# Kernel tuning notes

Measured on AMD Instinct MI355X. Metric: run time of the kernel, lower is better.

## Reference

```python
import jax, jax.numpy as jnp
import numpy as np

EMBED_DIM = 768
NUM_HEADS = 12
HEAD_DIM = EMBED_DIM // NUM_HEADS
MLP_RATIO = 4.0
HIDDEN_DIM = int(EMBED_DIM * MLP_RATIO)
B, N = 8, 1024


def setup_inputs() -> dict:
    key = jax.random.key(0)
    ks = jax.random.split(key, 12)
    d = EMBED_DIM
    h = HIDDEN_DIM
    s = lambda fan_in: 1.0 / np.sqrt(fan_in)
    return {
        "x": jax.random.normal(ks[0], (B, N, d), dtype=jnp.float32),
        "ln1_w": jnp.ones((d,), jnp.float32),
        "ln1_b": jnp.zeros((d,), jnp.float32),
        "qkv_w": jax.random.normal(ks[1], (3 * d, d), jnp.float32) * s(d),
        "qkv_b": jnp.zeros((3 * d,), jnp.float32),
        "proj_w": jax.random.normal(ks[2], (d, d), jnp.float32) * s(d),
        "proj_b": jnp.zeros((d,), jnp.float32),
        "ln2_w": jnp.ones((d,), jnp.float32),
        "ln2_b": jnp.zeros((d,), jnp.float32),
        "fc1_w": jax.random.normal(ks[3], (h, d), jnp.float32) * s(d),
        "fc1_b": jnp.zeros((h,), jnp.float32),
        "fc2_w": jax.random.normal(ks[4], (d, h), jnp.float32) * s(h),
        "fc2_b": jnp.zeros((d,), jnp.float32),
    }


def _layernorm(x, w, b, eps=1e-5):
    mu = jnp.mean(x, axis=-1, keepdims=True)
    var = jnp.var(x, axis=-1, keepdims=True)
    return (x - mu) * jax.lax.rsqrt(var + eps) * w + b


def _attention(x, qkv_w, qkv_b, proj_w, proj_b):
    b, n, c = x.shape
    qkv = x @ qkv_w.T + qkv_b  # [B, N, 3C]
    qkv = qkv.reshape(b, n, 3, NUM_HEADS, HEAD_DIM)
    q, k, v = jnp.moveaxis(qkv, 2, 0)  # each [B, N, H, Dh]
    scale = HEAD_DIM ** -0.5
    attn = jnp.einsum("bqhd,bkhd->bhqk", q, k) * scale  # [B, H, N, N]
    attn = jax.nn.softmax(attn, axis=-1)
    out = jnp.einsum("bhqk,bkhd->bqhd", attn, v).reshape(b, n, c)
    return out @ proj_w.T + proj_b


def reference(x, ln1_w, ln1_b, qkv_w, qkv_b, proj_w, proj_b,
              ln2_w, ln2_b, fc1_w, fc1_b, fc2_w, fc2_b):
    x = x + _attention(_layernorm(x, ln1_w, ln1_b), qkv_w, qkv_b, proj_w, proj_b)
    h = _layernorm(x, ln2_w, ln2_b)
    h = jax.nn.gelu(h @ fc1_w.T + fc1_b, approximate=False)
    x = x + (h @ fc2_w.T + fc2_b)
    return x
```

## Files before the change

kernel.cpp:

```cpp
#include <hip/hip_runtime.h>
#include <hip/hip_bf16.h>
#include <math.h>

typedef __attribute__((ext_vector_type(8))) short bf16x8;
typedef __attribute__((ext_vector_type(4))) float f32x4;
typedef unsigned short ushort_t;

#define GLOAD(srcp, dstp) __builtin_amdgcn_global_load_lds((const __attribute__((address_space(1))) void*)(srcp), (__attribute__((address_space(3))) void*)(dstp), 16, 0, 0)

__device__ inline ushort_t f2bfn(float f){
  union{ __bf16 h; ushort_t u; } c;
  c.h = (__bf16)f;
  return c.u;
}

__global__ __launch_bounds__(256) void cvt_all(const float* __restrict__ q, const float* __restrict__ p,
                                               const float* __restrict__ f1, const float* __restrict__ f2w,
                                               ushort_t* __restrict__ dq, ushort_t* __restrict__ dp,
                                               ushort_t* __restrict__ d1, ushort_t* __restrict__ d2){
  int i4 = blockIdx.x*256 + threadIdx.x;
  const float* src; ushort_t* dst; int off;
  if(i4 < 442368){ src=q;  dst=dq; off=i4; }
  else if(i4 < 589824){ src=p;  dst=dp; off=i4-442368; }
  else if(i4 < 1179648){ src=f1; dst=d1; off=i4-589824; }
  else { src=f2w; dst=d2; off=i4-1179648; }
  int i = off*4;
  float4 v = *(const float4*)(src+i);
  ushort4 o; o.x=f2bfn(v.x); o.y=f2bfn(v.y); o.z=f2bfn(v.z); o.w=f2bfn(v.w);
  *(ushort4*)(dst+i) = o;
}

__global__ __launch_bounds__(192) void ln_kernel(const float* __restrict__ x, const float* __restrict__ w,
                                                 const float* __restrict__ b, ushort_t* __restrict__ out){
  int row = blockIdx.x, t = threadIdx.x;
  const float4 v = *(const float4*)(x + (size_t)row*768 + t*4);
  float s  = v.x+v.y+v.z+v.w;
  float s2 = v.x*v.x+v.y*v.y+v.z*v.z+v.w*v.w;
  for(int m=1;m<64;m<<=1){ s += __shfl_xor(s,m,64); s2 += __shfl_xor(s2,m,64); }
  __shared__ float ls[3], ls2[3];
  int wv_ = t>>6;
  if((t&63)==0){ ls[wv_]=s; ls2[wv_]=s2; }
  __syncthreads();
  s = ls[0]+ls[1]+ls[2]; s2 = ls2[0]+ls2[1]+ls2[2];
  float mu = s*(1.f/768.f);
  float var = s2*(1.f/768.f) - mu*mu;
  float rs = rsqrtf(var + 1e-5f);
  float4 wv4 = *(const float4*)(w + t*4);
  float4 bv4 = *(const float4*)(b + t*4);
  ushort4 o;
  o.x = f2bfn((v.x-mu)*rs*wv4.x + bv4.x);
  o.y = f2bfn((v.y-mu)*rs*wv4.y + bv4.y);
  o.z = f2bfn((v.z-mu)*rs*wv4.z + bv4.z);
  o.w = f2bfn((v.w-mu)*rs*wv4.w + bv4.w);
  *(ushort4*)(out + (size_t)row*768 + t*4) = o;
}

template<int EPI>
__device__ __forceinline__
void gemm8_body(const ushort_t* __restrict__ A, const ushort_t* __restrict__ BT,
                const float* __restrict__ bias, void* __restrict__ out,
                int K, int Nout, int nBN)
{
  __shared__ ushort_t lds[65536];
  ushort_t* As = lds;
  ushort_t* Bs = lds + 32768;
  const int tid = threadIdx.x;
  const int lane = tid & 63, wid = tid >> 6;
  const int wm = wid >> 2, wn = wid & 3;
  const int fq = lane >> 4, fr = lane & 15;

  const int nwg = (int)gridDim.x;
  const int bid = (int)blockIdx.x;
  const int wg = (bid & 7)*(nwg>>3) + (bid>>3);
  const int bm0 = (wg / nBN) << 8;
  const int bn0 = (wg % nBN) << 8;

  const int srow0 = tid >> 2;
  const int srow1 = 128 + srow0;
  const int sgc = ((tid & 3) ^ ((srow0 >> 1) & 3)) << 3;

  auto stageA = [&](int slot, int tile, int kh){
    const int k0 = (tile<<6) + (kh<<5);
    GLOAD(A + (size_t)(bm0 + srow0)*K + k0 + sgc, As + slot*8192 + (wid*64)*8);
    GLOAD(A + (size_t)(bm0 + srow1)*K + k0 + sgc, As + slot*8192 + (512 + wid*64)*8);
  };
  auto stageB = [&](int slot, int tile, int kh){
    const int k0 = (tile<<6) + (kh<<5);
    GLOAD(BT + (size_t)(bn0 + srow0)*K + k0 + sgc, Bs + slot*8192 + (wid*64)*8);
    GLOAD(BT + (size_t)(bn0 + srow1)*K + k0 + sgc, Bs + slot*8192 + (512 + wid*64)*8);
  };

  int aoff[8], boff[4];
  #pragma unroll
  for(int m=0;m<8;m++){ int r = wm*128 + m*16 + fr; aoff[m] = r*32 + ((fq ^ ((r>>1)&3))<<3); }
  #pragma unroll
  for(int n=0;n<4;n++){ int r = wn*64  + n*16 + fr; boff[n] = r*32 + ((fq ^ ((r>>1)&3))<<3); }

  f32x4 acc[8][4];
  #pragma unroll
  for(int m=0;m<8;m++)
    #pragma unroll
    for(int n=0;n<4;n++) acc[m][n] = (f32x4){0.f,0.f,0.f,0.f};

  const int NT = K >> 6;
  stageA(0,0,0); stageB(0,0,0);
  stageA(1,0,1); stageB(1,0,1);
  stageA(2,1,0); stageB(2,1,0);
  asm volatile("s_waitcnt vmcnt(4)" ::: "memory");
  __builtin_amdgcn_s_barrier();

  for(int g=0; g<NT; ++g){
    const int par = g & 1;
    const int sl0 = par*2, sl1 = par*2 + 1;
    const int osl1 = (par^1)*2 + 1;
    bf16x8 a[8], b0, b1;

    #pragma unroll
    for(int m=0;m<8;m++) a[m] = *(const bf16x8*)(As + sl0*8192 + aoff[m]);
    b0 = *(const bf16x8*)(Bs + sl0*8192 + boff[0]);
    b1 = *(const bf16x8*)(Bs + sl0*8192 + boff[1]);
    if(g+1 < NT) stageA(osl1, g+1, 1);
    __builtin_amdgcn_s_barrier();
    asm volatile("s_waitcnt lgkmcnt(0)" ::: "memory");
    __builtin_amdgcn_s_setprio(1);
    #pragma unroll
    for(int m=0;m<8;m++){
      acc[m][0] = __builtin_amdgcn_mfma_f32_16x16x32_bf16(a[m], b0, acc[m][0], 0,0,0);
      acc[m][1] = __builtin_amdgcn_mfma_f32_16x16x32_bf16(a[m], b1, acc[m][1], 0,0,0);
    }
    __builtin_amdgcn_s_setprio(0);

    b0 = *(const bf16x8*)(Bs + sl0*8192 + boff[2]);
    b1 = *(const bf16x8*)(Bs + sl0*8192 + boff[3]);
    if(g+1 < NT) stageB(osl1, g+1, 1);
    __builtin_amdgcn_s_barrier();
    asm volatile("s_waitcnt lgkmcnt(0)" ::: "memory");
    __builtin_amdgcn_s_setprio(1);
    #pragma unroll
    for(int m=0;m<8;m++){
      acc[m][2] = __builtin_amdgcn_mfma_f32_16x16x32_bf16(a[m], b0, acc[m][2], 0,0,0);
      acc[m][3] = __builtin_amdgcn_mfma_f32_16x16x32_bf16(a[m], b1, acc[m][3], 0,0,0);
    }
    __builtin_amdgcn_s_setprio(0);
    if(g+1 < NT){ asm volatile("s_waitcnt vmcnt(8)" ::: "memory"); }
    else        { asm volatile("s_waitcnt vmcnt(0)" ::: "memory"); }
    __builtin_amdgcn_s_barrier();

    #pragma unroll
    for(int m=0;m<8;m++) a[m] = *(const bf16x8*)(As + sl1*8192 + aoff[m]);
    b0 = *(const bf16x8*)(Bs + sl1*8192 + boff[0]);
    b1 = *(const bf16x8*)(Bs + sl1*8192 + boff[1]);
    if(g+2 < NT) stageA(sl0, g+2, 0);
    __builtin_amdgcn_s_barrier();
    asm volatile("s_waitcnt lgkmcnt(0)" ::: "memory");
    __builtin_amdgcn_s_setprio(1);
    #pragma unroll
    for(int m=0;m<8;m++){
      acc[m][0] = __builtin_amdgcn_mfma_f32_16x16x32_bf16(a[m], b0, acc[m][0], 0,0,0);
      acc[m][1] = __builtin_amdgcn_mfma_f32_16x16x32_bf16(a[m], b1, acc[m][1], 0,0,0);
    }
    __builtin_amdgcn_s_setprio(0);

    b0 = *(const bf16x8*)(Bs + sl1*8192 + boff[2]);
    b1 = *(const bf16x8*)(Bs + sl1*8192 + boff[3]);
    if(g+2 < NT) stageB(sl0, g+2, 0);
    __builtin_amdgcn_s_barrier();
    asm volatile("s_waitcnt lgkmcnt(0)" ::: "memory");
    __builtin_amdgcn_s_setprio(1);
    #pragma unroll
    for(int m=0;m<8;m++){
      acc[m][2] = __builtin_amdgcn_mfma_f32_16x16x32_bf16(a[m], b0, acc[m][2], 0,0,0);
      acc[m][3] = __builtin_amdgcn_mfma_f32_16x16x32_bf16(a[m], b1, acc[m][3], 0,0,0);
    }
    __builtin_amdgcn_s_setprio(0);
    if(g+2 < NT)      { asm volatile("s_waitcnt vmcnt(8)" ::: "memory"); }
    else if(g+1 < NT) { asm volatile("s_waitcnt vmcnt(4)" ::: "memory"); }
    else              { asm volatile("s_waitcnt vmcnt(0)" ::: "memory"); }
    __builtin_amdgcn_s_barrier();
  }

  __syncthreads();
  const float qscale = 0.18033688f;
  const bool isQ = (EPI==0) && (bn0 < 768);
  #pragma unroll
  for(int m=0;m<8;m++){
    #pragma unroll
    for(int n=0;n<4;n++){
      int colL = wn*64 + n*16 + fr;
      float bv = bias[bn0 + colL];
      #pragma unroll
      for(int j=0;j<4;j++){
        int rowL = wm*128 + m*16 + fq*4 + j;
        float v = acc[m][n][j] + bv;
        if constexpr(EPI==2){
          float u = fminf(v*(1.0f + 0.044715f*v*v), 40.f);
          float e = exp2f(2.3020052f*u);
          v = v*e/(1.0f+e);
        }
        if(isQ) v *= qscale;
        lds[rowL*256 + (colL ^ (((rowL>>2)&3)<<4))] = f2bfn(v);
      }
    }
  }
  __syncthreads();
  const bool isV = (EPI==0) && (bn0 >= 1536);
  if(!isV){
    #pragma unroll 4
    for(int p=0;p<16;p++){
      int flat = tid + p*512;
      int row = flat>>5;
      int c8  = flat&31;
      int col = c8*8;
      bf16x8 v8 = *(const bf16x8*)&lds[row*256 + (col ^ (((row>>2)&3)<<4))];
      int rg = bm0 + row;
      if constexpr(EPI==0){
        int colg = bn0 + col;
        int which = colg >= 768 ? 1 : 0;
        int rem = colg - which*768;
        int hh = rem>>6, dh = rem&63;
        int bb = rg>>10, np = rg&1023;
        *(bf16x8*)&((ushort_t*)out)[(((size_t)(which*96 + bb*12 + hh)*1024 + np)<<6) + dh] = v8;
      } else {
        *(bf16x8*)&((ushort_t*)out)[(size_t)rg*(size_t)Nout + bn0 + col] = v8;
      }
    }
  } else {
    #pragma unroll 4
    for(int p=0;p<16;p++){
      int flat = tid + p*512;
      int dL = flat>>5;
      int t8 = (flat&31)*8;
      ushort_t tmp[8];
      #pragma unroll
      for(int i=0;i<8;i++){
        int row = t8 + i;
        tmp[i] = lds[row*256 + (dL ^ (((row>>2)&3)<<4))];
      }
      int dg = bn0 - 1536 + dL;
      int hh = dg>>6, dh = dg&63;
      int tok0 = bm0 + t8;
      int bb = tok0>>10, np = tok0&1023;
      *(bf16x8*)&((ushort_t*)out)[((size_t)(192 + bb*12 + hh)*65536) + dh*1024 + np] = *(bf16x8*)tmp;
    }
  }
}

__global__ __launch_bounds__(512, 2)
void qkv_gemm8(const ushort_t* __restrict__ A, const ushort_t* __restrict__ BT,
               const float* __restrict__ bias, void* __restrict__ out, int K, int Nout, int nBN)
{ gemm8_body<0>(A, BT, bias, out, K, Nout, nBN); }

__global__ __launch_bounds__(512, 2)
void fc1_gemm8(const ushort_t* __restrict__ A, const ushort_t* __restrict__ BT,
               const float* __restrict__ bias, void* __restrict__ out, int K, int Nout, int nBN)
{ gemm8_body<2>(A, BT, bias, out, K, Nout, nBN); }

__device__ __forceinline__
void gemm_body_epi1(const ushort_t* __restrict__ A, const ushort_t* __restrict__ BT,
                    const float* __restrict__ bias, const float* __restrict__ resid,
                    float* __restrict__ out, int K, int nBN)
{
  __shared__ ushort_t Asm[4][64*32];
  __shared__ ushort_t Bsm[4][128*32];
  const int nwg = (int)gridDim.x;
  const int bid = (int)blockIdx.x;
  const int wg = (bid & 7)*(nwg>>3) + (bid>>3);
  const int bm0 = (wg / nBN) * 64;
  const int bn0 = (wg % nBN) * 128;
  const int tid = threadIdx.x;
  const int lane = tid & 63;
  const int wid = tid >> 6;
  const int wn = wid;
  const int fq = lane>>4, fr = lane&15;

  const int rA = tid>>2;
  const int cAs = ((tid&3) ^ ((rA>>1)&3))<<3;
  const int r0 = wid*32 + (lane>>2);
  const int r1 = r0 + 16;
  const int cBs = ((lane&3) ^ ((r0>>1)&3))<<3;

  f32x4 acc[4][2];
  for(int m=0;m<4;m++) for(int n=0;n<2;n++) acc[m][n] = (f32x4){0.f,0.f,0.f,0.f};

  auto STAGE = [&](int buf, int k0){
    GLOAD(A  + (size_t)(bm0+rA)*K + k0 + cAs, &Asm[buf][wid*512]);
    GLOAD(BT + (size_t)(bn0+r0)*K + k0 + cBs, &Bsm[buf][(wid*2)*512]);
    GLOAD(BT + (size_t)(bn0+r1)*K + k0 + cBs, &Bsm[buf][(wid*2+1)*512]);
  };

  int aoff[4], boff[2];
  #pragma unroll
  for(int m=0;m<4;m++){ int r = m*16 + fr; aoff[m] = r*32 + ((fq ^ ((r>>1)&3))<<3); }
  #pragma unroll
  for(int n=0;n<2;n++){ int r = wn*32 + n*16 + fr; boff[n] = r*32 + ((fq ^ ((r>>1)&3))<<3); }

  const int NT = K>>5;
  STAGE(0, 0);
  STAGE(1, 32);
  STAGE(2, 64);
  asm volatile("s_waitcnt vmcnt(6)" ::: "memory");
  __builtin_amdgcn_s_barrier();

  int cur = 0;
  for(int kt=0; kt<NT; ++kt){
    if(kt+3 < NT) STAGE((cur+3)&3, (kt+3)<<5);
    bf16x8 af[4], bfr[2];
    #pragma unroll
    for(int m=0;m<4;m++)
      af[m] = *(const bf16x8*)(&Asm[cur][aoff[m]]);
    #pragma unroll
    for(int n=0;n<2;n++)
      bfr[n] = *(const bf16x8*)(&Bsm[cur][boff[n]]);
    #pragma unroll
    for(int m=0;m<4;m++)
      #pragma unroll
      for(int n=0;n<2;n++)
        acc[m][n] = __builtin_amdgcn_mfma_f32_16x16x32_bf16(af[m], bfr[n], acc[m][n], 0,0,0);
    if(kt+1 < NT){
      if(kt+3 < NT)      { asm volatile("s_waitcnt vmcnt(6)" ::: "memory"); }
      else if(kt+2 < NT) { asm volatile("s_waitcnt vmcnt(3)" ::: "memory"); }
      else               { asm volatile("s_waitcnt vmcnt(0)" ::: "memory"); }
      __builtin_amdgcn_s_barrier();
    }
    cur = (cur+1)&3;
  }

  for(int m=0;m<4;m++){
    int row0 = bm0 + m*16 + fq*4;
    for(int n=0;n<2;n++){
      int col = bn0 + wn*32 + n*16 + fr;
      float bv = bias[col];
      for(int j=0;j<4;j++){
        int r = row0 + j;
        float v = acc[m][n][j] + bv + resid[(size_t)r*768 + col];
        out[(size_t)r*768 + col] = v;
      }
    }
  }
}

__global__ __launch_bounds__(256)
void proj_gemm(const ushort_t* __restrict__ A, const ushort_t* __restrict__ BT,
               const float* __restrict__ bias, const float* __restrict__ resid,
               float* __restrict__ out, int K, int nBN)
{ gemm_body_epi1(A, BT, bias, resid, out, K, nBN); }

__global__ __launch_bounds__(256)
void fc2_gemm(const ushort_t* __restrict__ A, const ushort_t* __restrict__ BT,
              const float* __restrict__ bias, const float* __restrict__ resid,
              float* __restrict__ out, int K, int nBN)
{ gemm_body_epi1(A, BT, bias, resid, out, K, nBN); }

__global__ __launch_bounds__(256)
void attn_kernel(const ushort_t* __restrict__ qkv, ushort_t* __restrict__ outp)
{
  __shared__ ushort_t Ksm[2][64*72];
  __shared__ ushort_t Vt[2][64*72];
  __shared__ ushort_t Psm[4][16*72];
  const int bh = blockIdx.y;
  const int q0 = blockIdx.x*64;
  const int tid = threadIdx.x, lane = tid&63, wid = tid>>6;
  const int fq = lane>>4, fr = lane&15;
  const ushort_t* Qb = qkv + ((size_t)bh*1024)*64;
  const ushort_t* Kb = qkv + ((size_t)(96 + bh)*1024)*64;
  const ushort_t* Vb = qkv + ((size_t)(192 + bh))*65536;

  bf16x8 ones;
  #pragma unroll
  for(int i=0;i<8;i++) ones[i] = (short)0x3F80;

  bf16x8 qf[2];
  {
    int qr = q0 + wid*16 + fr;
    qf[0] = *(const bf16x8*)(Qb + (size_t)qr*64 +      fq*8);
    qf[1] = *(const bf16x8*)(Qb + (size_t)qr*64 + 32 + fq*8);
  }
  f32x4 o[4];
  for(int dt=0;dt<4;dt++) o[dt] = (f32x4){0.f,0.f,0.f,0.f};
  float lrun[4];
  for(int j=0;j<4;j++) lrun[j]=0.f;

  const int sr = tid>>3, sc = (tid&7)*8;

  bf16x8 k0r = *(const bf16x8*)(Kb + (size_t)sr*64 + sc);
  bf16x8 k1r = *(const bf16x8*)(Kb + (size_t)(sr+32)*64 + sc);
  bf16x8 v0r = *(const bf16x8*)(Vb + (size_t)sr*1024 + sc);
  bf16x8 v1r = *(const bf16x8*)(Vb + (size_t)(sr+32)*1024 + sc);
  *(bf16x8*)(Ksm[0] + sr*72 + sc)      = k0r;
  *(bf16x8*)(Ksm[0] + (sr+32)*72 + sc) = k1r;
  *(bf16x8*)(Vt[0]  + sr*72 + sc)      = v0r;
  *(bf16x8*)(Vt[0]  + (sr+32)*72 + sc) = v1r;

  int cur = 0;
  for(int kt=0; kt<16; kt++){
    __syncthreads();
    if(kt+1 < 16){
      int kv1 = (kt+1)*64;
      k0r = *(const bf16x8*)(Kb + (size_t)(kv1+sr)*64 + sc);
      k1r = *(const bf16x8*)(Kb + (size_t)(kv1+sr+32)*64 + sc);
      v0r = *(const bf16x8*)(Vb + (size_t)sr*1024 + kv1 + sc);
      v1r = *(const bf16x8*)(Vb + (size_t)(sr+32)*1024 + kv1 + sc);
    }

    f32x4 s[4];
    for(int ct=0;ct<4;ct++){
      bf16x8 kf0 = *(const bf16x8*)(Ksm[cur] + (ct*16 + fr)*72 +      fq*8);
      bf16x8 kf1 = *(const bf16x8*)(Ksm[cur] + (ct*16 + fr)*72 + 32 + fq*8);
      f32x4 z = (f32x4){0.f,0.f,0.f,0.f};
      z = __builtin_amdgcn_mfma_f32_16x16x32_bf16(qf[0], kf0, z, 0,0,0);
      z = __builtin_amdgcn_mfma_f32_16x16x32_bf16(qf[1], kf1, z, 0,0,0);
      s[ct] = z;
    }

    #pragma unroll
    for(int ct=0;ct<4;ct++){
      #pragma unroll
      for(int j=0;j<4;j++){
        float p = exp2f(s[ct][j]);
        int g = (ct*2 + (fr>>3)) ^ fq;
        Psm[wid][(fq*4 + j)*72 + g*8 + (fr&7)] = f2bfn(p);
      }
    }

    bf16x8 pf[2];
    {
      int key = (fr>>2)&3;
      pf[0] = *(const bf16x8*)(&Psm[wid][fr*72 + ((0*4+fq)^key)*8]);
      pf[1] = *(const bf16x8*)(&Psm[wid][fr*72 + ((1*4+fq)^key)*8]);
    }
    f32x4 o5 = (f32x4){0.f,0.f,0.f,0.f};
    o5 = __builtin_amdgcn_mfma_f32_16x16x32_bf16(pf[0], ones, o5, 0,0,0);
    o5 = __builtin_amdgcn_mfma_f32_16x16x32_bf16(pf[1], ones, o5, 0,0,0);
    #pragma unroll
    for(int j=0;j<4;j++) lrun[j] += o5[j];

    for(int dt=0;dt<4;dt++){
      for(int kc=0;kc<2;kc++){
        bf16x8 vf = *(const bf16x8*)(Vt[cur] + (dt*16 + fr)*72 + kc*32 + fq*8);
        o[dt] = __builtin_amdgcn_mfma_f32_16x16x32_bf16(pf[kc], vf, o[dt], 0,0,0);
      }
    }

    if(kt+1 < 16){
      *(bf16x8*)(Ksm[cur^1] + sr*72 + sc)      = k0r;
      *(bf16x8*)(Ksm[cur^1] + (sr+32)*72 + sc) = k1r;
      *(bf16x8*)(Vt[cur^1]  + sr*72 + sc)      = v0r;
      *(bf16x8*)(Vt[cur^1]  + (sr+32)*72 + sc) = v1r;
    }
    cur ^= 1;
  }

  int b = bh/12, h = bh%12;
  for(int dt=0;dt<4;dt++){
    for(int j=0;j<4;j++){
      int qr = q0 + wid*16 + fq*4 + j;
      float v = o[dt][j] / lrun[j];
      outp[(size_t)(b*1024 + qr)*768 + h*64 + dt*16 + fr] = f2bfn(v);
    }
  }
}

extern "C" void kernel_launch(void* const* d_in, const int* in_sizes, int n_in,
                              void* d_out, int out_size, void* d_ws, size_t ws_size,
                              hipStream_t stream)
{
  const float* x     = (const float*)d_in[0];
  const float* ln1w  = (const float*)d_in[1];
  const float* ln1b  = (const float*)d_in[2];
  const float* qkvw  = (const float*)d_in[3];
  const float* qkvb  = (const float*)d_in[4];
  const float* projw = (const float*)d_in[5];
  const float* projb = (const float*)d_in[6];
  const float* ln2w  = (const float*)d_in[7];
  const float* ln2b  = (const float*)d_in[8];
  const float* fc1w  = (const float*)d_in[9];
  const float* fc1b  = (const float*)d_in[10];
  const float* fc2w  = (const float*)d_in[11];
  const float* fc2b  = (const float*)d_in[12];

  char* ws = (char*)d_ws;
  size_t off = 0;
  auto alloc = [&](size_t bytes){ char* p = ws + off; off += (bytes + 255) & ~255ULL; return p; };
  ushort_t* wq = (ushort_t*)alloc((size_t)2304*768*2);
  ushort_t* wp = (ushort_t*)alloc((size_t)768*768*2);
  ushort_t* w1 = (ushort_t*)alloc((size_t)3072*768*2);
  ushort_t* w2 = (ushort_t*)alloc((size_t)768*3072*2);
  ushort_t* lnbuf  = (ushort_t*)alloc((size_t)8192*768*2);
  ushort_t* qkvbuf = (ushort_t*)alloc((size_t)3*96*1024*64*2);
  ushort_t* attno  = (ushort_t*)alloc((size_t)8192*768*2);
  ushort_t* hbuf   = qkvbuf;
  float* x1 = (float*)d_out;

  cvt_all<<<6912, 256, 0, stream>>>(qkvw, projw, fc1w, fc2w, wq, wp, w1, w2);
  ln_kernel<<<8192, 192, 0, stream>>>(x, ln1w, ln1b, lnbuf);
  qkv_gemm8<<<288, 512, 0, stream>>>(lnbuf, wq, qkvb, qkvbuf, 768, 2304, 9);
  attn_kernel<<<dim3(16,96), 256, 0, stream>>>(qkvbuf, attno);
  proj_gemm<<<768, 256, 0, stream>>>(attno, wp, projb, x, x1, 768, 6);
  ln_kernel<<<8192, 192, 0, stream>>>(x1, ln2w, ln2b, lnbuf);
  fc1_gemm8<<<384, 512, 0, stream>>>(lnbuf, w1, fc1b, hbuf, 768, 3072, 12);
  fc2_gemm<<<768, 256, 0, stream>>>(hbuf, w2, fc2b, x1, (float*)d_out, 3072, 6);
}
```

Baseline: 310.8 us.

## Halve GEMM LDS footprint with two-slot staging and split epilogue

Shrinks the shared-memory buffer for the QKV/FC1 GEMM from 128KB to 64KB. It drops the four-slot, two-tile-deep prefetch ring in favour of two fixed slots, each refilled once per iteration with a full vmcnt(0) wait. The epilogue now writes its bf16 tile through LDS in two 128-row halves so it fits the smaller buffer. The aim is to let two 512-thread workgroups share a CU (matching launch_bounds(512,2)), at the cost of a shallower prefetch that can expose global-load latency, plus extra barriers in the epilogue.

```diff
diff --git a/kernel.cpp b/kernel.cpp
--- a/kernel.cpp
+++ b/kernel.cpp
@@ -61,9 +61,9 @@
                 const float* __restrict__ bias, void* __restrict__ out,
                 int K, int Nout, int nBN)
 {
-  __shared__ ushort_t lds[65536];
+  __shared__ ushort_t lds[32768];
   ushort_t* As = lds;
-  ushort_t* Bs = lds + 32768;
+  ushort_t* Bs = lds + 16384;
   const int tid = threadIdx.x;
   const int lane = tid & 63, wid = tid >> 6;
   const int wm = wid >> 2, wn = wid & 3;
@@ -105,21 +105,17 @@
   const int NT = K >> 6;
   stageA(0,0,0); stageB(0,0,0);
   stageA(1,0,1); stageB(1,0,1);
-  stageA(2,1,0); stageB(2,1,0);
   asm volatile("s_waitcnt vmcnt(4)" ::: "memory");
   __builtin_amdgcn_s_barrier();
 
   for(int g=0; g<NT; ++g){
-    const int par = g & 1;
-    const int sl0 = par*2, sl1 = par*2 + 1;
-    const int osl1 = (par^1)*2 + 1;
     bf16x8 a[8], b0, b1;
 
     #pragma unroll
-    for(int m=0;m<8;m++) a[m] = *(const bf16x8*)(As + sl0*8192 + aoff[m]);
-    b0 = *(const bf16x8*)(Bs + sl0*8192 + boff[0]);
-    b1 = *(const bf16x8*)(Bs + sl0*8192 + boff[1]);
-    if(g+1 < NT) stageA(osl1, g+1, 1);
+    for(int m=0;m<8;m++) a[m] = *(const bf16x8*)(As + aoff[m]);
+    b0 = *(const bf16x8*)(Bs + boff[0]);
+    b1 = *(const bf16x8*)(Bs + boff[1]);
+    if(g >= 1){ stageA(1, g, 1); stageB(1, g, 1); }
     __builtin_amdgcn_s_barrier();
     asm volatile("s_waitcnt lgkmcnt(0)" ::: "memory");
     __builtin_amdgcn_s_setprio(1);
@@ -130,9 +126,8 @@
     }
     __builtin_amdgcn_s_setprio(0);
 
-    b0 = *(const bf16x8*)(Bs + sl0*8192 + boff[2]);
-    b1 = *(const bf16x8*)(Bs + sl0*8192 + boff[3]);
-    if(g+1 < NT) stageB(osl1, g+1, 1);
+    b0 = *(const bf16x8*)(Bs + boff[2]);
+    b1 = *(const bf16x8*)(Bs + boff[3]);
     __builtin_amdgcn_s_barrier();
     asm volatile("s_waitcnt lgkmcnt(0)" ::: "memory");
     __builtin_amdgcn_s_setprio(1);
@@ -142,15 +137,14 @@
       acc[m][3] = __builtin_amdgcn_mfma_f32_16x16x32_bf16(a[m], b1, acc[m][3], 0,0,0);
     }
     __builtin_amdgcn_s_setprio(0);
-    if(g+1 < NT){ asm volatile("s_waitcnt vmcnt(8)" ::: "memory"); }
-    else        { asm volatile("s_waitcnt vmcnt(0)" ::: "memory"); }
-    __builtin_amdgcn_s_barrier();
-
-    #pragma unroll
-    for(int m=0;m<8;m++) a[m] = *(const bf16x8*)(As + sl1*8192 + aoff[m]);
-    b0 = *(const bf16x8*)(Bs + sl1*8192 + boff[0]);
-    b1 = *(const bf16x8*)(Bs + sl1*8192 + boff[1]);
-    if(g+2 < NT) stageA(sl0, g+2, 0);
+    asm volatile("s_waitcnt vmcnt(0)" ::: "memory");
+    __builtin_amdgcn_s_barrier();
+
+    #pragma unroll
+    for(int m=0;m<8;m++) a[m] = *(const bf16x8*)(As + 8192 + aoff[m]);
+    b0 = *(const bf16x8*)(Bs + 8192 + boff[0]);
+    b1 = *(const bf16x8*)(Bs + 8192 + boff[1]);
+    if(g+1 < NT){ stageA(0, g+1, 0); stageB(0, g+1, 0); }
     __builtin_amdgcn_s_barrier();
     asm volatile("s_waitcnt lgkmcnt(0)" ::: "memory");
     __builtin_amdgcn_s_setprio(1);
@@ -161,9 +155,8 @@
     }
     __builtin_amdgcn_s_setprio(0);
 
-    b0 = *(const bf16x8*)(Bs + sl1*8192 + boff[2]);
-    b1 = *(const bf16x8*)(Bs + sl1*8192 + boff[3]);
-    if(g+2 < NT) stageB(sl0, g+2, 0);
+    b0 = *(const bf16x8*)(Bs + 8192 + boff[2]);
+    b1 = *(const bf16x8*)(Bs + 8192 + boff[3]);
     __builtin_amdgcn_s_barrier();
     asm volatile("s_waitcnt lgkmcnt(0)" ::: "memory");
     __builtin_amdgcn_s_setprio(1);
@@ -173,74 +166,76 @@
       acc[m][3] = __builtin_amdgcn_mfma_f32_16x16x32_bf16(a[m], b1, acc[m][3], 0,0,0);
     }
     __builtin_amdgcn_s_setprio(0);
-    if(g+2 < NT)      { asm volatile("s_waitcnt vmcnt(8)" ::: "memory"); }
-    else if(g+1 < NT) { asm volatile("s_waitcnt vmcnt(4)" ::: "memory"); }
-    else              { asm volatile("s_waitcnt vmcnt(0)" ::: "memory"); }
-    __builtin_amdgcn_s_barrier();
-  }
-
-  __syncthreads();
+    asm volatile("s_waitcnt vmcnt(0)" ::: "memory");
+    __builtin_amdgcn_s_barrier();
+  }
+
   const float qscale = 0.18033688f;
   const bool isQ = (EPI==0) && (bn0 < 768);
-  #pragma unroll
-  for(int m=0;m<8;m++){
-    #pragma unroll
-    for(int n=0;n<4;n++){
-      int colL = wn*64 + n*16 + fr;
-      float bv = bias[bn0 + colL];
+  const bool isV = (EPI==0) && (bn0 >= 1536);
+  for(int h=0; h<2; ++h){
+    __syncthreads();
+    if(wm == h){
       #pragma unroll
-      for(int j=0;j<4;j++){
-        int rowL = wm*128 + m*16 + fq*4 + j;
-        float v = acc[m][n][j] + bv;
-        if constexpr(EPI==2){
-          float u = fminf(v*(1.0f + 0.044715f*v*v), 40.f);
-          float e = exp2f(2.3020052f*u);
-          v = v*e/(1.0f+e);
+      for(int m=0;m<8;m++){
+        #pragma unroll
+        for(int n=0;n<4;n++){
+          int colL = wn*64 + n*16 + fr;
+          float bv = bias[bn0 + colL];
+          #pragma unroll
+          for(int j=0;j<4;j++){
+            int rowL = wm*128 + m*16 + fq*4 + j;
+            int lr = rowL & 127;
+            float v = acc[m][n][j] + bv;
+            if constexpr(EPI==2){
+              float u = fminf(v*(1.0f + 0.044715f*v*v), 40.f);
+              float e = exp2f(2.3020052f*u);
+              v = v*e/(1.0f+e);
+            }
+            if(isQ) v *= qscale;
+            lds[lr*256 + (colL ^ (((lr>>2)&3)<<4))] = f2bfn(v);
+          }
         }
-        if(isQ) v *= qscale;
-        lds[rowL*256 + (colL ^ (((rowL>>2)&3)<<4))] = f2bfn(v);
-      }
-    }
-  }
-  __syncthreads();
-  const bool isV = (EPI==0) && (bn0 >= 1536);
-  if(!isV){
-    #pragma unroll 4
-    for(int p=0;p<16;p++){
-      int flat = tid + p*512;
-      int row = flat>>5;
-      int c8  = flat&31;
-      int col = c8*8;
-      bf16x8 v8 = *(const bf16x8*)&lds[row*256 + (col ^ (((row>>2)&3)<<4))];
-      int rg = bm0 + row;
-      if constexpr(EPI==0){
-        int colg = bn0 + col;
-        int which = colg >= 768 ? 1 : 0;
-        int rem = colg - which*768;
-        int hh = rem>>6, dh = rem&63;
-        int bb = rg>>10, np = rg&1023;
-        *(bf16x8*)&((ushort_t*)out)[(((size_t)(which*96 + bb*12 + hh)*1024 + np)<<6) + dh] = v8;
-      } else {
-        *(bf16x8*)&((ushort_t*)out)[(size_t)rg*(size_t)Nout + bn0 + col] = v8;
-      }
-    }
-  } else {
-    #pragma unroll 4
-    for(int p=0;p<16;p++){
-      int flat = tid + p*512;
-      int dL = flat>>5;
-      int t8 = (flat&31)*8;
-      ushort_t tmp[8];
-      #pragma unroll
-      for(int i=0;i<8;i++){
-        int row = t8 + i;
-        tmp[i] = lds[row*256 + (dL ^ (((row>>2)&3)<<4))];
-      }
-      int dg = bn0 - 1536 + dL;
-      int hh = dg>>6, dh = dg&63;
-      int tok0 = bm0 + t8;
-      int bb = tok0>>10, np = tok0&1023;
-      *(bf16x8*)&((ushort_t*)out)[((size_t)(192 + bb*12 + hh)*65536) + dh*1024 + np] = *(bf16x8*)tmp;
+      }
+    }
+    __syncthreads();
+    if(!isV){
+      #pragma unroll 4
+      for(int p=0;p<8;p++){
+        int flat = tid + p*512;
+        int row = flat>>5;
+        int col = (flat&31)*8;
+        bf16x8 v8 = *(const bf16x8*)&lds[row*256 + (col ^ (((row>>2)&3)<<4))];
+        int rg = bm0 + h*128 + row;
+        if constexpr(EPI==0){
+          int colg = bn0 + col;
+          int which = colg >= 768 ? 1 : 0;
+          int rem = colg - which*768;
+          int hh = rem>>6, dh = rem&63;
+          int bb = rg>>10, np = rg&1023;
+          *(bf16x8*)&((ushort_t*)out)[(((size_t)(which*96 + bb*12 + hh)*1024 + np)<<6) + dh] = v8;
+        } else {
+          *(bf16x8*)&((ushort_t*)out)[(size_t)rg*(size_t)Nout + bn0 + col] = v8;
+        }
+      }
+    } else {
+      #pragma unroll 4
+      for(int p=0;p<8;p++){
+        int flat = tid + p*512;
+        int dL = flat>>4;
+        int t8 = (flat&15)*8;
+        ushort_t tmp[8];
+        #pragma unroll
+        for(int i=0;i<8;i++){
+          int row = t8 + i;
+          tmp[i] = lds[row*256 + (dL ^ (((row>>2)&3)<<4))];
+        }
+        int dg = bn0 - 1536 + dL;
+        int hh = dg>>6, dh = dg&63;
+        int tok0 = bm0 + h*128 + t8;
+        int bb = tok0>>10, np = tok0&1023;
+        *(bf16x8*)&((ushort_t*)out)[((size_t)(192 + bb*12 + hh)*65536) + dh*1024 + np] = *(bf16x8*)tmp;
+      }
     }
   }
 }
```

Result: slower. 319.2 us (+2.7%).
